# Performance work log

Hardware: AMD Instinct MI355X
Metric: run time of the kernel (lower is better)

Reference implementation:

```python
import jax, jax.numpy as jnp
import numpy as np

D_MODEL = 1024
STATE = 16

def setup_inputs() -> dict:
    key = jax.random.key(0)
    ks = jax.random.split(key, 7)
    x = jax.random.normal(ks[0], (4, 4096, D_MODEL), dtype=jnp.float32)
    A_log = jax.random.normal(ks[1], (STATE,), dtype=jnp.float32)
    B = jax.random.normal(ks[2], (STATE, D_MODEL), dtype=jnp.float32) * 0.05
    C = jax.random.normal(ks[3], (D_MODEL, STATE), dtype=jnp.float32) * 0.05
    D = jax.random.normal(ks[4], (D_MODEL,), dtype=jnp.float32)
    W_delta = jax.random.normal(ks[5], (D_MODEL, D_MODEL), dtype=jnp.float32) * 0.02
    b_delta = jax.random.normal(ks[6], (D_MODEL,), dtype=jnp.float32) * 0.02
    return {"x": x, "A_log": A_log, "B": B, "C": C, "D": D,
            "W_delta": W_delta, "b_delta": b_delta}

def reference(x, A_log, B, C, D, W_delta, b_delta):
    # delta: softplus(Linear(x)).mean(-1) -> (b, l)
    delta = jax.nn.softplus(jnp.einsum('bld,ed->ble', x, W_delta) + b_delta).mean(-1)
    A = -jnp.exp(A_log)                         # (n,)
    Bx = jnp.einsum('bld,nd->bln', x, B)        # (b, l, n)
    dA = jnp.exp(delta[..., None] * A)          # (b, l, n)
    dBx = delta[..., None] * Bx                 # (b, l, n)

    def step(h, inp):
        dA_t, dBx_t = inp                       # (b, n) each
        h = dA_t * h + dBx_t
        return h, h

    h0 = jnp.zeros((x.shape[0], A_log.shape[0]), dtype=x.dtype)
    _, hs = jax.lax.scan(step, h0, (jnp.swapaxes(dA, 0, 1), jnp.swapaxes(dBx, 0, 1)))
    hs = jnp.swapaxes(hs, 0, 1)                 # (b, l, n)
    y = jnp.einsum('bln,dn->bld', hs, C) + D * x
    return y
```

## Files before the change

kernel.cpp:

```cpp
#include <hip/hip_runtime.h>
#include <hip/hip_bf16.h>
#include <stdint.h>

#define DM 1024
#define NS 16
#define LSEQ 4096
#define NB 4
#define MTOT (NB*LSEQ)
#define NC 128
#define LC 32

typedef __attribute__((ext_vector_type(8))) short bf16x8;
typedef __attribute__((ext_vector_type(4))) float f32x4;

__device__ __forceinline__ unsigned short f2bf(float f) {
    unsigned int u = __float_as_uint(f);
    unsigned int r = (u + 0x7FFFu + ((u >> 16) & 1u)) >> 16;
    return (unsigned short)r;
}

__device__ __forceinline__ float bf2f(unsigned short u) {
    return __uint_as_float(((unsigned int)u) << 16);
}

__device__ __forceinline__ float softplus_f(float v) {
    return v > 15.f ? v : __logf(1.f + __expf(v));
}

__device__ __forceinline__ void gload_lds16(const void* g, void* l) {
    __builtin_amdgcn_global_load_lds(
        (const __attribute__((address_space(1))) unsigned int*)g,
        (__attribute__((address_space(3))) unsigned int*)l, 16, 0, 0);
}

__global__ __launch_bounds__(256) void pre_kernel(
    const float4* __restrict__ x4, const float4* __restrict__ W4,
    const float4* __restrict__ B4, ushort4* __restrict__ xb4,
    ushort4* __restrict__ wb4, ushort4* __restrict__ bbf4,
    float* __restrict__ delta_raw)
{
    int bid = blockIdx.x, t = threadIdx.x;
    if (bid < 16384) {
        size_t i = (size_t)bid * 256 + t;
        float4 v = x4[i];
        ushort4 o; o.x = f2bf(v.x); o.y = f2bf(v.y); o.z = f2bf(v.z); o.w = f2bf(v.w);
        xb4[i] = o;
    } else if (bid < 17408) {
        int i = (bid - 16384) * 256 + t;
        float4 v = W4[i];
        ushort4 o; o.x = f2bf(v.x); o.y = f2bf(v.y); o.z = f2bf(v.z); o.w = f2bf(v.w);
        wb4[i] = o;
    } else if (bid < 17424) {
        int i = (bid - 17408) * 256 + t;
        float4 v = B4[i];
        ushort4 o; o.x = f2bf(v.x); o.y = f2bf(v.y); o.z = f2bf(v.z); o.w = f2bf(v.w);
        bbf4[i] = o;
    } else {
        int i = (bid - 17424) * 256 + t;
        ((float4*)delta_raw)[i] = (float4){0.f, 0.f, 0.f, 0.f};
    }
}

__global__ __launch_bounds__(512) void gemm_delta(
    const unsigned short* __restrict__ xb, const unsigned short* __restrict__ wb,
    const float* __restrict__ b_delta, float* __restrict__ delta_raw)
{
    __shared__ char lds[131072];
    int bid = blockIdx.x;
    int swz = (bid & 7) * 32 + (bid >> 3);
    int mb = swz >> 2, nb = swz & 3;
    int row0 = mb * 256, e0 = nb * 256;
    int tid = threadIdx.x;
    int lane = tid & 63, w = tid >> 6;
    int wr = w >> 2, wc = w & 3;
    int lm = lane & 15, lk = lane >> 4;

    int colsw = ((lane & 7) * 8) ^ ((lane >> 3) << 3);
    int rsub = lane >> 3;

    const unsigned short* pA[4];
    const unsigned short* pB[4];
    #pragma unroll
    for (int j = 0; j < 4; ++j) {
        int region = w * 4 + j;
        int r0 = region * 8 + rsub;
        pA[j] = xb + (size_t)(row0 + r0) * DM + colsw;
        pB[j] = wb + (size_t)(e0  + r0) * DM + colsw;
    }

    int sterm = (lm & 7) << 4;
    int off0 = (lk * 16) ^ sterm;
    int off1 = (64 + lk * 16) ^ sterm;
    int aBase = (wr * 128 + lm) * 128;
    int bBase = 32768 + (wc * 64 + lm) * 128;

    f32x4 acc[8][4];
    #pragma unroll
    for (int m = 0; m < 8; ++m)
        #pragma unroll
        for (int n = 0; n < 4; ++n)
            acc[m][n] = (f32x4){0.f, 0.f, 0.f, 0.f};

#define STAGE(BUF, KOFF) do { \
    _Pragma("unroll") \
    for (int j = 0; j < 4; ++j) { \
        int region = w * 4 + j; \
        gload_lds16(pA[j] + (KOFF), lds + (BUF) + region * 1024); \
        gload_lds16(pB[j] + (KOFF), lds + (BUF) + 32768 + region * 1024); \
    } } while (0)

#define COMPUTE(BUF) do { \
    bf16x8 bq[4][2]; \
    _Pragma("unroll") \
    for (int n = 0; n < 4; ++n) { \
        bq[n][0] = *(const bf16x8*)(lds + (BUF) + bBase + n * 2048 + off0); \
        bq[n][1] = *(const bf16x8*)(lds + (BUF) + bBase + n * 2048 + off1); \
    } \
    __builtin_amdgcn_s_setprio(1); \
    _Pragma("unroll") \
    for (int m = 0; m < 8; ++m) { \
        bf16x8 a0 = *(const bf16x8*)(lds + (BUF) + aBase + m * 2048 + off0); \
        bf16x8 a1 = *(const bf16x8*)(lds + (BUF) + aBase + m * 2048 + off1); \
        _Pragma("unroll") \
        for (int n = 0; n < 4; ++n) { \
            acc[m][n] = __builtin_amdgcn_mfma_f32_16x16x32_bf16(a0, bq[n][0], acc[m][n], 0, 0, 0); \
            acc[m][n] = __builtin_amdgcn_mfma_f32_16x16x32_bf16(a1, bq[n][1], acc[m][n], 0, 0, 0); \
        } \
    } \
    __builtin_amdgcn_s_setprio(0); \
} while (0)

#define KSTEP(CUR, NXT, KOFF) do { \
    STAGE(NXT, KOFF); \
    asm volatile("s_waitcnt vmcnt(8)\n\ts_barrier" ::: "memory"); \
    COMPUTE(CUR); \
    asm volatile("s_barrier" ::: "memory"); \
} while (0)

    STAGE(0, 0);
    int koff = 64;
    #pragma unroll 1
    for (int it = 0; it < 7; ++it) {
        KSTEP(0, 65536, koff);
        KSTEP(65536, 0, koff + 64);
        koff += 128;
    }
    KSTEP(0, 65536, 960);
    asm volatile("s_waitcnt vmcnt(0)\n\ts_barrier" ::: "memory");
    COMPUTE(65536);

#undef KSTEP
#undef COMPUTE
#undef STAGE

    float bd[4];
    #pragma unroll
    for (int n = 0; n < 4; ++n) bd[n] = b_delta[e0 + wc * 64 + n * 16 + lm];
    #pragma unroll
    for (int m = 0; m < 8; ++m) {
        #pragma unroll
        for (int r = 0; r < 4; ++r) {
            float s = 0.f;
            #pragma unroll
            for (int n = 0; n < 4; ++n) s += softplus_f(acc[m][n][r] + bd[n]);
            s += __shfl_xor(s, 1, 16);
            s += __shfl_xor(s, 2, 16);
            s += __shfl_xor(s, 4, 16);
            s += __shfl_xor(s, 8, 16);
            if (lm == 0) {
                int row = row0 + wr * 128 + m * 16 + lk * 4 + r;
                atomicAdd(&delta_raw[row], s);
            }
        }
    }
}

__global__ __launch_bounds__(256) void bx_mfma(
    const unsigned short* __restrict__ xb, const unsigned short* __restrict__ bbf,
    float* __restrict__ Bx)
{
    int tid = threadIdx.x, lane = tid & 63, w = tid >> 6;
    int rb = blockIdx.x * 4 + w;
    int r0 = rb * 16;
    int lm = lane & 15, lk = lane >> 4;
    const unsigned short* pa = xb + (size_t)(r0 + lm) * DM + lk * 8;
    const unsigned short* pb = bbf + (size_t)lm * DM + lk * 8;
    f32x4 acc = (f32x4){0.f, 0.f, 0.f, 0.f};
    #pragma unroll 4
    for (int k0 = 0; k0 < DM; k0 += 32) {
        bf16x8 a = *(const bf16x8*)(pa + k0);
        bf16x8 b = *(const bf16x8*)(pb + k0);
        acc = __builtin_amdgcn_mfma_f32_16x16x32_bf16(a, b, acc, 0, 0, 0);
    }
    #pragma unroll
    for (int r = 0; r < 4; ++r)
        Bx[(size_t)(r0 + lk * 4 + r) * NS + lm] = acc[r];
}

__global__ __launch_bounds__(64) void scan_pass1(
    const float* __restrict__ delta_raw, const float* __restrict__ Bx,
    const float* __restrict__ A_log, float* __restrict__ cP, float* __restrict__ cH)
{
    __shared__ float dl[LC];
    __shared__ float bxl[LC * NS];
    int bid = blockIdx.x;
    int b = bid >> 7, c = bid & 127;
    int l0 = c * LC;
    int t = threadIdx.x;
    size_t base = (size_t)b * LSEQ + l0;
    if (t < LC) dl[t] = delta_raw[base + t] * (1.f / 1024.f);
    const float4* src = (const float4*)(Bx + base * NS);
    float4* dst = (float4*)bxl;
    dst[t] = src[t];
    dst[t + 64] = src[t + 64];
    __syncthreads();
    if (t < NS) {
        float a = -__expf(A_log[t]);
        float P = 1.f, h = 0.f;
        #pragma unroll
        for (int s = 0; s < LC; ++s) {
            float dlt = dl[s];
            float dA = __expf(dlt * a);
            h = dA * h + dlt * bxl[s * NS + t];
            P *= dA;
        }
        int idx = (b * NC + c) * NS + t;
        cP[idx] = P; cH[idx] = h;
    }
}

__global__ __launch_bounds__(256) void y_kernel(
    const unsigned short* __restrict__ xb, const float* __restrict__ delta_raw,
    const float* __restrict__ Bx, const float* __restrict__ A_log,
    const float* __restrict__ cP, const float* __restrict__ cH,
    const float* __restrict__ C, const float* __restrict__ Dv, float* __restrict__ y)
{
    __shared__ float dl[LC];
    __shared__ float bxl[LC * NS];
    __shared__ float hsl[LC * NS];
    __shared__ float pbuf[NC * NS];
    __shared__ float hbuf[NC * NS];
    int bid = blockIdx.x;
    int b = bid >> 7, c = bid & 127;
    int l0 = c * LC;
    int t = threadIdx.x;
    size_t base = (size_t)b * LSEQ + l0;
    if (t < LC) dl[t] = delta_raw[base + t] * (1.f / 1024.f);
    if (t < 128) ((float4*)bxl)[t] = ((const float4*)(Bx + base * NS))[t];
    {
        const float4* p4 = (const float4*)(cP + (size_t)b * NC * NS);
        const float4* h4 = (const float4*)(cH + (size_t)b * NC * NS);
        ((float4*)pbuf)[t] = p4[t];         ((float4*)pbuf)[t + 256] = p4[t + 256];
        ((float4*)hbuf)[t] = h4[t];         ((float4*)hbuf)[t + 256] = h4[t + 256];
    }
    __syncthreads();
    if (t < NS) {
        float h = 0.f;
        for (int cc = 0; cc < c; ++cc) {
            int idx = cc * NS + t;
            h = pbuf[idx] * h + hbuf[idx];
        }
        float a = -__expf(A_log[t]);
        #pragma unroll
        for (int s = 0; s < LC; ++s) {
            float dlt = dl[s];
            float dA = __expf(dlt * a);
            h = dA * h + dlt * bxl[s * NS + t];
            hsl[s * NS + t] = h;
        }
    }
    __syncthreads();

    int d0 = t * 4;
    float cr[4][NS];
    #pragma unroll
    for (int dd = 0; dd < 4; ++dd)
        #pragma unroll
        for (int nn = 0; nn < 4; ++nn) {
            float4 c4 = ((const float4*)C)[((d0 + dd) * NS + nn * 4) >> 2];
            cr[dd][nn * 4 + 0] = c4.x; cr[dd][nn * 4 + 1] = c4.y;
            cr[dd][nn * 4 + 2] = c4.z; cr[dd][nn * 4 + 3] = c4.w;
        }
    float4 dv = ((const float4*)Dv)[t];
    const ushort4* xr = (const ushort4*)(xb + base * DM) + t;
    float4* yr = (float4*)(y + base * DM) + t;
    for (int s = 0; s < LC; ++s) {
        float hv[NS];
        #pragma unroll
        for (int n = 0; n < NS; ++n) hv[n] = hsl[s * NS + n];
        ushort4 xv4 = xr[s * 256];
        float4 o;
        o.x = dv.x * bf2f(xv4.x); o.y = dv.y * bf2f(xv4.y);
        o.z = dv.z * bf2f(xv4.z); o.w = dv.w * bf2f(xv4.w);
        #pragma unroll
        for (int n = 0; n < NS; ++n) {
            o.x += hv[n] * cr[0][n];
            o.y += hv[n] * cr[1][n];
            o.z += hv[n] * cr[2][n];
            o.w += hv[n] * cr[3][n];
        }
        yr[s * 256] = o;
    }
}

extern "C" void kernel_launch(void* const* d_in, const int* in_sizes, int n_in,
                              void* d_out, int out_size, void* d_ws, size_t ws_size,
                              hipStream_t stream)
{
    const float* x     = (const float*)d_in[0];
    const float* A_log = (const float*)d_in[1];
    const float* B     = (const float*)d_in[2];
    const float* C     = (const float*)d_in[3];
    const float* Dv    = (const float*)d_in[4];
    const float* Wd    = (const float*)d_in[5];
    const float* bd    = (const float*)d_in[6];
    float* y = (float*)d_out;

    char* ws = (char*)d_ws;
    unsigned short* xb = (unsigned short*)ws;
    unsigned short* wb = (unsigned short*)(ws + 33554432);
    float* delta_raw   = (float*)(ws + 35651584);
    float* Bx          = (float*)(ws + 35717120);
    float* cP          = (float*)(ws + 36765696);
    float* cH          = (float*)(ws + 36798464);
    unsigned short* bbf= (unsigned short*)(ws + 36831232);

    pre_kernel<<<17440, 256, 0, stream>>>((const float4*)x, (const float4*)Wd,
                                          (const float4*)B, (ushort4*)xb,
                                          (ushort4*)wb, (ushort4*)bbf, delta_raw);
    gemm_delta<<<256, 512, 0, stream>>>(xb, wb, bd, delta_raw);
    bx_mfma<<<256, 256, 0, stream>>>(xb, bbf, Bx);
    scan_pass1<<<NB * NC, 64, 0, stream>>>(delta_raw, Bx, A_log, cP, cH);
    y_kernel<<<NB * NC, 256, 0, stream>>>(xb, delta_raw, Bx, A_log, cP, cH, C, Dv, y);
}
```

Baseline: 97.97 us.

## Split GEMM K-tile into four phases interleaving global-to-LDS loads with MFMA

Breaks each K-tile of the delta GEMM main loop into four phases. Each phase issues one quarter of the next tile's global-to-LDS loads, reads two A row-blocks from LDS, and runs the matching MFMAs. B fragments are loaded once per tile in the first phase, with a tighter vmcnt wait. The aim is a finer-grained overlap of memory traffic with matrix compute and less register pressure from the A fragments. The cost is many more workgroup barriers per K-tile.

```diff
diff --git a/kernel.cpp b/kernel.cpp
--- a/kernel.cpp
+++ b/kernel.cpp
@@ -101,57 +101,62 @@
         for (int n = 0; n < 4; ++n)
             acc[m][n] = (f32x4){0.f, 0.f, 0.f, 0.f};
 
-#define STAGE(BUF, KOFF) do { \
-    _Pragma("unroll") \
-    for (int j = 0; j < 4; ++j) { \
-        int region = w * 4 + j; \
-        gload_lds16(pA[j] + (KOFF), lds + (BUF) + region * 1024); \
-        gload_lds16(pB[j] + (KOFF), lds + (BUF) + 32768 + region * 1024); \
-    } } while (0)
-
-#define COMPUTE(BUF) do { \
-    bf16x8 bq[4][2]; \
+    bf16x8 bq[4][2];
+
+#define STAGE_Q(BUF, Q, KOFF) do { \
+    gload_lds16(pA[Q] + (KOFF), lds + (BUF) + ((w * 4 + (Q)) * 1024)); \
+    gload_lds16(pB[Q] + (KOFF), lds + (BUF) + 32768 + ((w * 4 + (Q)) * 1024)); \
+} while (0)
+
+#define PHASE(CUR, NXT, KOFF, STG, Q) do { \
+    if (STG) STAGE_Q(NXT, Q, KOFF); \
+    if ((Q) == 0) { \
+        if (STG) asm volatile("s_waitcnt vmcnt(2)\n\ts_barrier" ::: "memory"); \
+        else     asm volatile("s_waitcnt vmcnt(0)\n\ts_barrier" ::: "memory"); \
+        _Pragma("unroll") \
+        for (int n = 0; n < 4; ++n) { \
+            bq[n][0] = *(const bf16x8*)(lds + (CUR) + bBase + n * 2048 + off0); \
+            bq[n][1] = *(const bf16x8*)(lds + (CUR) + bBase + n * 2048 + off1); \
+        } \
+    } \
+    bf16x8 a0 = *(const bf16x8*)(lds + (CUR) + aBase + (2*(Q)) * 2048 + off0); \
+    bf16x8 a1 = *(const bf16x8*)(lds + (CUR) + aBase + (2*(Q)) * 2048 + off1); \
+    bf16x8 a2 = *(const bf16x8*)(lds + (CUR) + aBase + (2*(Q)+1) * 2048 + off0); \
+    bf16x8 a3 = *(const bf16x8*)(lds + (CUR) + aBase + (2*(Q)+1) * 2048 + off1); \
+    asm volatile("s_barrier" ::: "memory"); \
+    __builtin_amdgcn_s_setprio(1); \
     _Pragma("unroll") \
     for (int n = 0; n < 4; ++n) { \
-        bq[n][0] = *(const bf16x8*)(lds + (BUF) + bBase + n * 2048 + off0); \
-        bq[n][1] = *(const bf16x8*)(lds + (BUF) + bBase + n * 2048 + off1); \
-    } \
-    __builtin_amdgcn_s_setprio(1); \
-    _Pragma("unroll") \
-    for (int m = 0; m < 8; ++m) { \
-        bf16x8 a0 = *(const bf16x8*)(lds + (BUF) + aBase + m * 2048 + off0); \
-        bf16x8 a1 = *(const bf16x8*)(lds + (BUF) + aBase + m * 2048 + off1); \
-        _Pragma("unroll") \
-        for (int n = 0; n < 4; ++n) { \
-            acc[m][n] = __builtin_amdgcn_mfma_f32_16x16x32_bf16(a0, bq[n][0], acc[m][n], 0, 0, 0); \
-            acc[m][n] = __builtin_amdgcn_mfma_f32_16x16x32_bf16(a1, bq[n][1], acc[m][n], 0, 0, 0); \
-        } \
+        acc[2*(Q)][n]   = __builtin_amdgcn_mfma_f32_16x16x32_bf16(a0, bq[n][0], acc[2*(Q)][n], 0, 0, 0); \
+        acc[2*(Q)][n]   = __builtin_amdgcn_mfma_f32_16x16x32_bf16(a1, bq[n][1], acc[2*(Q)][n], 0, 0, 0); \
+        acc[2*(Q)+1][n] = __builtin_amdgcn_mfma_f32_16x16x32_bf16(a2, bq[n][0], acc[2*(Q)+1][n], 0, 0, 0); \
+        acc[2*(Q)+1][n] = __builtin_amdgcn_mfma_f32_16x16x32_bf16(a3, bq[n][1], acc[2*(Q)+1][n], 0, 0, 0); \
     } \
     __builtin_amdgcn_s_setprio(0); \
-} while (0)
-
-#define KSTEP(CUR, NXT, KOFF) do { \
-    STAGE(NXT, KOFF); \
-    asm volatile("s_waitcnt vmcnt(8)\n\ts_barrier" ::: "memory"); \
-    COMPUTE(CUR); \
     asm volatile("s_barrier" ::: "memory"); \
 } while (0)
 
-    STAGE(0, 0);
+#define KTILE(CUR, NXT, KOFF, STG) do { \
+    PHASE(CUR, NXT, KOFF, STG, 0); \
+    PHASE(CUR, NXT, KOFF, STG, 1); \
+    PHASE(CUR, NXT, KOFF, STG, 2); \
+    PHASE(CUR, NXT, KOFF, STG, 3); \
+} while (0)
+
+    STAGE_Q(0, 0, 0); STAGE_Q(0, 1, 0); STAGE_Q(0, 2, 0); STAGE_Q(0, 3, 0);
     int koff = 64;
     #pragma unroll 1
     for (int it = 0; it < 7; ++it) {
-        KSTEP(0, 65536, koff);
-        KSTEP(65536, 0, koff + 64);
+        KTILE(0,     65536, koff,      true);
+        KTILE(65536, 0,     koff + 64, true);
         koff += 128;
     }
-    KSTEP(0, 65536, 960);
-    asm volatile("s_waitcnt vmcnt(0)\n\ts_barrier" ::: "memory");
-    COMPUTE(65536);
-
-#undef KSTEP
-#undef COMPUTE
-#undef STAGE
+    KTILE(0, 65536, 960, true);
+    KTILE(65536, 0, 0, false);
+
+#undef KTILE
+#undef PHASE
+#undef STAGE_Q
 
     float bd[4];
     #pragma unroll
```

Result: faster. 94.09 us (-4.0%).
